# Optimization experiments

Hardware: AMD Instinct MI355X
Metric: run time of the kernel (lower is better)

## Reference

```python
import jax, jax.numpy as jnp
import numpy as np
import math

D = 2048            # fc_feat_size (hardcoded sqrt(2048) scale in source)
IMAGES = 20         # images_per_person
NEIGHBOR = 5        # neighbor_size (sliding window width)
T = IMAGES - NEIGHBOR + 1   # number of windows = 16
SCALE = 1.0 / math.sqrt(2048.0)


def _attention(x, Wq, bq, Wk, bk, Wv, bv):
    # x: [N, L, D] -> [N, L, D]; bmm-softmax-bmm as in source
    q = x @ Wq.T + bq
    k = x @ Wk.T + bk
    v = x @ Wv.T + bv
    dot = jnp.einsum('nld,nmd->nlm', q, k) * SCALE
    w = jax.nn.softmax(dot, axis=-1)
    return jnp.einsum('nlm,nmd->nld', w, v)


def _lstm_final(x, Wih, Whh, bih, bhh):
    # PyTorch-convention LSTM (gates i,f,g,o); x: [N, L, D] -> final hidden [N, H]
    N = x.shape[0]
    H = Whh.shape[1]
    xg = x @ Wih.T + (bih + bhh)   # [N, L, 4H] precompute input projections

    def step(carry, xt):
        h, c = carry
        gates = xt + h @ Whh.T
        i, f, g, o = jnp.split(gates, 4, axis=-1)
        c = jax.nn.sigmoid(f) * c + jax.nn.sigmoid(i) * jnp.tanh(g)
        h = jax.nn.sigmoid(o) * jnp.tanh(c)
        return (h, c), None

    init = (jnp.zeros((N, H), x.dtype), jnp.zeros((N, H), x.dtype))
    (h, _), _ = jax.lax.scan(step, init, jnp.swapaxes(xg, 0, 1))
    return h


def _layernorm(x, g, b, eps=1e-5):
    mu = jnp.mean(x, axis=-1, keepdims=True)
    var = jnp.var(x, axis=-1, keepdims=True)
    return (x - mu) * jax.lax.rsqrt(var + eps) * g + b


def setup_inputs() -> dict:
    key = jax.random.key(0)
    ks = iter(jax.random.split(key, 32))
    s = 0.02
    p = {}
    p['fc_feats'] = jax.random.normal(next(ks), (64, IMAGES, D), jnp.float32)
    for pre in ('nsa', 'sa'):
        for nm in ('Wq', 'Wk', 'Wv'):
            p[f'{pre}_{nm}'] = jax.random.normal(next(ks), (D, D), jnp.float32) * s
        for nm in ('bq', 'bk', 'bv'):
            p[f'{pre}_{nm}'] = jnp.zeros((D,), jnp.float32)
        p[f'{pre}_Wih'] = jax.random.normal(next(ks), (4 * D, D), jnp.float32) * s
        p[f'{pre}_Whh'] = jax.random.normal(next(ks), (4 * D, D), jnp.float32) * s
        p[f'{pre}_bih'] = jnp.zeros((4 * D,), jnp.float32)
        p[f'{pre}_bhh'] = jnp.zeros((4 * D,), jnp.float32)
    p['ln_g'] = jnp.ones((D,), jnp.float32)
    p['ln_b'] = jnp.zeros((D,), jnp.float32)
    return p


def reference(fc_feats,
              nsa_Wq, nsa_Wk, nsa_Wv, nsa_bq, nsa_bk, nsa_bv,
              nsa_Wih, nsa_Whh, nsa_bih, nsa_bhh,
              sa_Wq, sa_Wk, sa_Wv, sa_bq, sa_bk, sa_bv,
              sa_Wih, sa_Whh, sa_bih, sa_bhh,
              ln_g, ln_b):
    B = fc_feats.shape[0]
    # Sliding windows: window t covers images [t, t+NEIGHBOR) -> [B, T, W, D]
    idx = jnp.arange(T)[:, None] + jnp.arange(NEIGHBOR)[None, :]
    windows = fc_feats[:, idx]                       # [B, T, W, D]
    wflat = windows.reshape(B * T, NEIGHBOR, D)
    # NeighboringSelfAttention: attention within window + LSTM final state
    att = _attention(wflat, nsa_Wq, nsa_bq, nsa_Wk, nsa_bk, nsa_Wv, nsa_bv)
    nsa = _lstm_final(att, nsa_Wih, nsa_Whh, nsa_bih, nsa_bhh)  # [B*T, D]
    nsa_feats = nsa.reshape(B, T, D)
    new_nsa_feats = _layernorm(nsa_feats, ln_g, ln_b)
    # SelfAttention over the T window summaries + LSTM final state
    att2 = _attention(new_nsa_feats, sa_Wq, sa_bq, sa_Wk, sa_bk, sa_Wv, sa_bv)
    sa_feats = _lstm_final(att2, sa_Wih, sa_Whh, sa_bih, sa_bhh)  # [B, D]
    return (sa_feats, new_nsa_feats)
```

## Files before the change

### kernel.cpp

```cpp
#include <hip/hip_runtime.h>
#include <hip/hip_bf16.h>

typedef unsigned int  u32;
typedef unsigned short u16;

typedef __bf16 bf16x8 __attribute__((ext_vector_type(8)));
typedef float  f32x4  __attribute__((ext_vector_type(4)));

#define D2048 2048
#define SCALE 0.022097086912079612f

__device__ __forceinline__ u32 f2bfbits(float f) {
    u32 u = __float_as_uint(f);
    return (u + 0x7FFFu + ((u >> 16) & 1u)) >> 16;
}
__device__ __forceinline__ u32 pack2(float a, float b) {
    return f2bfbits(a) | (f2bfbits(b) << 16);
}
__device__ __forceinline__ float bf2f(u32 h) {
    return __uint_as_float(h << 16);
}
__device__ __forceinline__ void unpack8(uint4 v, float* f) {
    f[0] = bf2f(v.x & 0xFFFFu); f[1] = bf2f(v.x >> 16);
    f[2] = bf2f(v.y & 0xFFFFu); f[3] = bf2f(v.y >> 16);
// ... 6 lines not shown
    float e = __expf(2.f * x);
    return (e - 1.f) / (e + 1.f);
}

__device__ __forceinline__ void gload_lds16(const u16* g, u16* l) {
    __builtin_amdgcn_global_load_lds(
        (const __attribute__((address_space(1))) unsigned int*)g,
        (__attribute__((address_space(3))) unsigned int*)l,
        16, 0, 0);
}

struct CvtArgs {
    const float* src[8];
    u16*         dst[8];
    int          n4[8];
    int          nseg;
};
__global__ __launch_bounds__(256) void cvt_multi(CvtArgs a) {
    int stride = gridDim.x * 256;
    for (int s = 0; s < a.nseg; ++s) {
        const float4* S = reinterpret_cast<const float4*>(a.src[s]);
        uint2*        D = reinterpret_cast<uint2*>(a.dst[s]);
        int n4 = a.n4[s];
        for (int i = blockIdx.x * 256 + threadIdx.x; i < n4; i += stride) {
            float4 v = S[i];
            uint2 p;
            p.x = pack2(v.x, v.y);
            p.y = pack2(v.z, v.w);
            D[i] = p;
        }
    }
}

template <int SPLITK, bool OUT_BF16>
__global__ __launch_bounds__(512, 2) void gemm256(const u16* __restrict__ A, int lda,
                                                  const u16* __restrict__ B,
                                                  void* __restrict__ C0,
                                                  void* __restrict__ C1,
                                                  int M, int N, int K) {
    __shared__ u16 Ab[2][16384];
    __shared__ u16 Bb[2][16384];

    const int tid  = threadIdx.x;
    const int lane = tid & 63;
    const int wid  = tid >> 6;
    const int wm   = wid >> 2;
    const int wn   = wid & 3;
    const int l15  = lane & 15, l4 = lane >> 4;
    const int rowBase = blockIdx.y * 256;
    const int colBase = blockIdx.x * 256;
    const int kseg = K / SPLITK;
    const int kBeg = (SPLITK > 1) ? (int)blockIdx.z * kseg : 0;

    const int srow8 = lane >> 3;
    const int scw   = ((lane & 7) ^ srow8) * 8;
    const u16* gA = A + (size_t)(rowBase + wid * 8 + srow8) * lda + kBeg + scw;
    const u16* gB = B + (size_t)(colBase + wid * 8 + srow8) * (size_t)K + kBeg + scw;
    const int ldsW = wid * 512;

#define STAGE_A(buf, koff, q) \
    gload_lds16(gA + (size_t)((q) * 64) * lda + (koff), &Ab[buf][(q) * 4096 + ldsW])
#define STAGE_B(buf, koff, q) \
    gload_lds16(gB + (size_t)((q) * 64) * (size_t)K + (koff), &Bb[buf][(q) * 4096 + ldsW])

    f32x4 acc[8][4];
#pragma unroll
    for (int m = 0; m < 8; m++)
#pragma unroll
        for (int n = 0; n < 4; n++) acc[m][n] = f32x4{0.f, 0.f, 0.f, 0.f};

    const int nt = kseg >> 6;

#pragma unroll
    for (int q = 0; q < 4; ++q) { STAGE_A(0, 0, q); STAGE_B(0, 0, q); }

    const int swzA = (l15 & 7);

    for (int t = 0; t < nt; ++t) {
        const int cur = t & 1;
        const int nxt = cur ^ 1;
        const int kN  = (t + 1) << 6;
        const bool more = (t + 1 < nt);

        if (more) {
            STAGE_A(nxt, kN, 0);
            STAGE_A(nxt, kN, 1);
            asm volatile("s_waitcnt vmcnt(2)" ::: "memory");
        } else {
            asm volatile("s_waitcnt vmcnt(0)" ::: "memory");
        }
        __builtin_amdgcn_s_barrier();

        bf16x8 bfrag[4][2];
#pragma unroll
        for (int n = 0; n < 4; ++n)
#pragma unroll
            for (int kk = 0; kk < 2; ++kk)
                bfrag[n][kk] = *reinterpret_cast<const bf16x8*>(
                    &Bb[cur][(wn * 64 + n * 16 + l15) * 64 +
                             (((kk * 4 + l4) ^ swzA) * 8)]);

#pragma unroll
        for (int p = 0; p < 4; ++p) {
            bf16x8 afr[2][2];
#pragma unroll
            for (int mi = 0; mi < 2; ++mi)
#pragma unroll
                for (int kk = 0; kk < 2; ++kk)
                    afr[mi][kk] = *reinterpret_cast<const bf16x8*>(
                        &Ab[cur][(wm * 128 + (p * 2 + mi) * 16 + l15) * 64 +
                                 (((kk * 4 + l4) ^ swzA) * 8)]);
            if (more) {
                if (p == 0)      { STAGE_A(nxt, kN, 2); STAGE_A(nxt, kN, 3); }
                else if (p == 1) { STAGE_B(nxt, kN, 0); STAGE_B(nxt, kN, 1); }
                else if (p == 2) { STAGE_B(nxt, kN, 2); STAGE_B(nxt, kN, 3); }
            }
            __builtin_amdgcn_s_barrier();
            __builtin_amdgcn_sched_barrier(0);
            __builtin_amdgcn_s_setprio(1);
#pragma unroll
            for (int kk = 0; kk < 2; ++kk)
#pragma unroll
                for (int mi = 0; mi < 2; ++mi)
#pragma unroll
                    for (int n = 0; n < 4; ++n)
                        acc[p * 2 + mi][n] = __builtin_amdgcn_mfma_f32_16x16x32_bf16(
                            afr[mi][kk], bfrag[n][kk], acc[p * 2 + mi][n], 0, 0, 0);
            __builtin_amdgcn_s_setprio(0);
            __builtin_amdgcn_sched_barrier(0);
            __builtin_amdgcn_s_barrier();
        }
    }
#undef STAGE_A
#undef STAGE_B

    float* fdst = (SPLITK > 1 && blockIdx.z) ? (float*)C1 : (float*)C0;
#pragma unroll
    for (int m = 0; m < 8; ++m) {
        int row0 = rowBase + wm * 128 + m * 16 + l4 * 4;
#pragma unroll
        for (int n = 0; n < 4; ++n) {
            int col = colBase + wn * 64 + n * 16 + l15;
#pragma unroll
            for (int rr = 0; rr < 4; ++rr) {
                if (OUT_BF16)
                    ((u16*)C0)[(size_t)(row0 + rr) * N + col] = (u16)f2bfbits(acc[m][n][rr]);
                else
                    fdst[(size_t)(row0 + rr) * N + col] = acc[m][n][rr];
            }
        }
    }
}

template <bool QKV3, bool HAS_BIAS, bool OUT_BF16>
__global__ __launch_bounds__(256) void gemm_bt(const u16* __restrict__ A, int lda,
                                               const u16* __restrict__ B0,
                                               const u16* __restrict__ B1,
                                               const u16* __restrict__ B2,
                                               const float* __restrict__ bias0,
                                               const float* __restrict__ bias1,
                                               const float* __restrict__ bias2,
                                               void* __restrict__ Cout,
                                               size_t zCstride,
                                               int M, int N, int K) {
    __shared__ u16 Abuf[2][128 * 64];
    __shared__ u16 Bbuf[2][128 * 64];

    const int tid  = threadIdx.x;
    const int lane = tid & 63;
    const int wave = tid >> 6;
    const int wr   = (wave >> 1) * 64;
    const int wc   = (wave & 1) * 64;
    const int rowBase = blockIdx.y * 128;
    const int colBase = blockIdx.x * 128;
    const int l15 = lane & 15, l4 = lane >> 4;
    const int srow = lane >> 3;
    const int scol = (lane & 7) * 8;

    const u16* B = B0;
    const float* bias = bias0;
    void* C = Cout;
    if (QKV3) {
        int z = blockIdx.z;
        B    = (z == 0) ? B0 : ((z == 1) ? B1 : B2);
        bias = (z == 0) ? bias0 : ((z == 1) ? bias1 : bias2);
        C    = OUT_BF16 ? (void*)((u16*)Cout + (size_t)z * zCstride)
                        : (void*)((float*)Cout + (size_t)z * zCstride);
    }

    const u16* ga = A + (size_t)(rowBase + wave * 32 + srow) * lda + scol;
    const u16* gb = B + (size_t)(colBase + wave * 32 + srow) * K + scol;
    const int ldsOff = (wave * 32) * 64;

    f32x4 acc[4][4];
#pragma unroll
    for (int i = 0; i < 4; i++)
#pragma unroll
        for (int j = 0; j < 4; j++) acc[i][j] = f32x4{0.f, 0.f, 0.f, 0.f};

    const int nt = K >> 6;

#pragma unroll
    for (int i = 0; i < 4; ++i) {
        gload_lds16(ga + (size_t)(i * 8) * lda, &Abuf[0][ldsOff + i * 8 * 64]);
        gload_lds16(gb + (size_t)(i * 8) * K,   &Bbuf[0][ldsOff + i * 8 * 64]);
    }

    for (int t = 0; t < nt; ++t) {
        const int cur = t & 1;
        if (t + 1 < nt) {
            const int k1 = (t + 1) << 6;
#pragma unroll
            for (int i = 0; i < 4; ++i) {
                gload_lds16(ga + (size_t)(i * 8) * lda + k1,
                            &Abuf[cur ^ 1][ldsOff + i * 8 * 64]);
                gload_lds16(gb + (size_t)(i * 8) * K + k1,
                            &Bbuf[cur ^ 1][ldsOff + i * 8 * 64]);
            }
            asm volatile("s_waitcnt vmcnt(8)" ::: "memory");
        } else {
            asm volatile("s_waitcnt vmcnt(0)" ::: "memory");
        }
        __builtin_amdgcn_s_barrier();
        __builtin_amdgcn_sched_barrier(0);
#pragma unroll
        for (int kk = 0; kk < 2; ++kk) {
            bf16x8 af[4], bfr[4];
#pragma unroll
            for (int i = 0; i < 4; i++) {
                af[i]  = *reinterpret_cast<const bf16x8*>(
                    &Abuf[cur][(wr + i * 16 + l15) * 64 + kk * 32 + l4 * 8]);
                bfr[i] = *reinterpret_cast<const bf16x8*>(
                    &Bbuf[cur][(wc + i * 16 + l15) * 64 + kk * 32 + l4 * 8]);
            }
#pragma unroll
            for (int i = 0; i < 4; i++)
#pragma unroll
                for (int j = 0; j < 4; j++)
                    acc[i][j] = __builtin_amdgcn_mfma_f32_16x16x32_bf16(af[i], bfr[j],
                                                                        acc[i][j], 0, 0, 0);
        }
        __builtin_amdgcn_sched_barrier(0);
        __builtin_amdgcn_s_barrier();
    }

#pragma unroll
    for (int i = 0; i < 4; i++) {
        int row0 = rowBase + wr + i * 16 + l4 * 4;
#pragma unroll
        for (int j = 0; j < 4; j++) {
            int col = colBase + wc + j * 16 + l15;
            float bv = HAS_BIAS ? bias[col] : 0.f;
#pragma unroll
            for (int rr = 0; rr < 4; rr++) {
                float val = acc[i][j][rr] + bv;
                if (OUT_BF16)
                    ((u16*)C)[(size_t)(row0 + rr) * N + col] = (u16)f2bfbits(val);
                else
                    ((float*)C)[(size_t)(row0 + rr) * N + col] = val;
            }
        }
    }
}

__global__ __launch_bounds__(256) void gemm_skinny64(const u16* __restrict__ A,
                                                     const u16* __restrict__ B,
                                                     float* __restrict__ part,
                                                     int N, int K) {
    __shared__ u16 Abuf[2][64 * 64];
    __shared__ u16 Bbuf[2][128 * 64];
    const int tid = threadIdx.x, lane = tid & 63, wave = tid >> 6;
    const int colBase = blockIdx.x * 128;
    const int kp = blockIdx.y;
    const int kseg = K >> 3;
    const int kBeg = kp * kseg;
    const int l15 = lane & 15, l4 = lane >> 4;
    const int srow = lane >> 3, scol = (lane & 7) * 8;

    const u16* ga = A + (size_t)(wave * 16 + srow) * K + scol + kBeg;
    const u16* gb = B + (size_t)(colBase + wave * 32 + srow) * K + scol + kBeg;
    const int laOff = (wave * 16) * 64;
    const int lbOff = (wave * 32) * 64;

    f32x4 acc[4][2];
#pragma unroll
    for (int i = 0; i < 4; i++)
#pragma unroll
        for (int j = 0; j < 2; j++) acc[i][j] = f32x4{0.f, 0.f, 0.f, 0.f};

    const int nt = kseg >> 6;

#pragma unroll
    for (int i = 0; i < 2; ++i)
        gload_lds16(ga + (size_t)(i * 8) * K, &Abuf[0][laOff + i * 8 * 64]);
#pragma unroll
    for (int i = 0; i < 4; ++i)
        gload_lds16(gb + (size_t)(i * 8) * K, &Bbuf[0][lbOff + i * 8 * 64]);

    for (int t = 0; t < nt; ++t) {
        const int cur = t & 1;
        if (t + 1 < nt) {
            const int k1 = (t + 1) << 6;
#pragma unroll
            for (int i = 0; i < 2; ++i)
                gload_lds16(ga + (size_t)(i * 8) * K + k1, &Abuf[cur ^ 1][laOff + i * 8 * 64]);
#pragma unroll
            for (int i = 0; i < 4; ++i)
                gload_lds16(gb + (size_t)(i * 8) * K + k1, &Bbuf[cur ^ 1][lbOff + i * 8 * 64]);
            asm volatile("s_waitcnt vmcnt(6)" ::: "memory");
        } else {
            asm volatile("s_waitcnt vmcnt(0)" ::: "memory");
        }
        __builtin_amdgcn_s_barrier();
        __builtin_amdgcn_sched_barrier(0);
#pragma unroll
        for (int kk = 0; kk < 2; ++kk) {
            bf16x8 af[4], bfr[2];
#pragma unroll
            for (int i = 0; i < 4; i++)
                af[i] = *reinterpret_cast<const bf16x8*>(
                    &Abuf[cur][(i * 16 + l15) * 64 + kk * 32 + l4 * 8]);
#pragma unroll
            for (int j = 0; j < 2; j++)
                bfr[j] = *reinterpret_cast<const bf16x8*>(
                    &Bbuf[cur][(wave * 32 + j * 16 + l15) * 64 + kk * 32 + l4 * 8]);
#pragma unroll
            for (int i = 0; i < 4; i++)
#pragma unroll
                for (int j = 0; j < 2; j++)
                    acc[i][j] = __builtin_amdgcn_mfma_f32_16x16x32_bf16(af[i], bfr[j],
                                                                        acc[i][j], 0, 0, 0);
        }
        __builtin_amdgcn_sched_barrier(0);
        __builtin_amdgcn_s_barrier();
    }

    float* cp = part + (size_t)kp * 64 * N;
#pragma unroll
    for (int i = 0; i < 4; i++) {
        int row0 = i * 16 + l4 * 4;
#pragma unroll
        for (int j = 0; j < 2; j++) {
            int col = colBase + wave * 32 + j * 16 + l15;
#pragma unroll
            for (int rr = 0; rr < 4; rr++)
                cp[(size_t)(row0 + rr) * N + col] = acc[i][j][rr];
        }
    }
}

__global__ __launch_bounds__(256) void attn_win5(const u16* __restrict__ q0,
                                                 const u16* __restrict__ k0,
                                                 const u16* __restrict__ v0,
                                                 u16* __restrict__ att) {
    int n = blockIdx.x;
    int b = n >> 4, t = n & 15;
    int tid = threadIdx.x, lane = tid & 63, wave = tid >> 6;
    int d0 = tid * 8;
    size_t base = (size_t)(b * 20 + t) * D2048;

    float qv[5][8];
#pragma unroll
    for (int i = 0; i < 5; i++) {
        uint4 v = *reinterpret_cast<const uint4*>(q0 + base + (size_t)i * D2048 + d0);
        unpack8(v, qv[i]);
    }
    float part[25];
#pragma unroll
    for (int p = 0; p < 25; p++) part[p] = 0.f;
#pragma unroll
    for (int m = 0; m < 5; m++) {
        float kv[8];
        uint4 v = *reinterpret_cast<const uint4*>(k0 + base + (size_t)m * D2048 + d0);
        unpack8(v, kv);
#pragma unroll
        for (int l = 0; l < 5; l++)
#pragma unroll
            for (int j = 0; j < 8; j++) part[l * 5 + m] += qv[l][j] * kv[j];
    }
#pragma unroll
    for (int p = 0; p < 25; p++) {
// ... 99 lines not shown
        float dv[16], mx = -1e30f;
#pragma unroll
        for (int m = 0; m < 16; m++) {
            dv[m] = (wred[0][m] + wred[1][m] + wred[2][m] + wred[3][m]) * SCALE;
            mx = fmaxf(mx, dv[m]);
        }
        float ssum = 0.f;
#pragma unroll
        for (int m = 0; m < 16; m++) { dv[m] = __expf(dv[m] - mx); ssum += dv[m]; }
        float inv = 1.f / ssum;
#pragma unroll
        for (int m = 0; m < 16; m++) wmat[m] = dv[m] * inv;
    }
    __syncthreads();

    float oacc[8];
#pragma unroll
    for (int j = 0; j < 8; j++) oacc[j] = 0.f;
#pragma unroll
    for (int m = 0; m < 16; m++) {
        float vv[8];
        uint4 v = *reinterpret_cast<const uint4*>(v2 + kbase + (size_t)m * D2048 + d0);
        unpack8(v, vv);
        float w = wmat[m];
#pragma unroll
        for (int j = 0; j < 8; j++) oacc[j] += w * vv[j];
    }
    uint4 p;
    p.x = pack2(oacc[0], oacc[1]);
    p.y = pack2(oacc[2], oacc[3]);
    p.z = pack2(oacc[4], oacc[5]);
    p.w = pack2(oacc[6], oacc[7]);
    *reinterpret_cast<uint4*>(att2 + (size_t)r * D2048 + d0) = p;
}

template <int NPARTS>
__global__ __launch_bounds__(256) void lstm_gate(const u16* __restrict__ xg,
                                                 int xg_stride,
                                                 const float* __restrict__ hWa,
                                                 const float* __restrict__ hWb,
                                                 const float* __restrict__ bih,
                                                 const float* __restrict__ bhh,
                                                 float* __restrict__ c,
                                                 float* __restrict__ h,
                                                 u16* __restrict__ hbf,
                                                 float* __restrict__ hout,
                                                 int rows) {
    int idx = blockIdx.x * 256 + threadIdx.x;
    int total = rows * 512;
    if (idx >= total) return;
    int n  = idx >> 9;
    int j4 = (idx & 511) * 4;

    const u16* xr = xg + (size_t)n * xg_stride + j4;
    float4 gi, gf, gg, go;
    {
        uint2 ri = *reinterpret_cast<const uint2*>(xr);
        uint2 rf = *reinterpret_cast<const uint2*>(xr + 2048);
        uint2 rg = *reinterpret_cast<const uint2*>(xr + 4096);
        uint2 ro = *reinterpret_cast<const uint2*>(xr + 6144);
        gi = {bf2f(ri.x & 0xFFFFu), bf2f(ri.x >> 16), bf2f(ri.y & 0xFFFFu), bf2f(ri.y >> 16)};
        gf = {bf2f(rf.x & 0xFFFFu), bf2f(rf.x >> 16), bf2f(rf.y & 0xFFFFu), bf2f(rf.y >> 16)};
        gg = {bf2f(rg.x & 0xFFFFu), bf2f(rg.x >> 16), bf2f(rg.y & 0xFFFFu), bf2f(rg.y >> 16)};
        go = {bf2f(ro.x & 0xFFFFu), bf2f(ro.x >> 16), bf2f(ro.y & 0xFFFFu), bf2f(ro.y >> 16)};
    }

    float4 bi1 = *reinterpret_cast<const float4*>(bih + j4);
    float4 bf1 = *reinterpret_cast<const float4*>(bih + 2048 + j4);
    float4 bg1 = *reinterpret_cast<const float4*>(bih + 4096 + j4);
    float4 bo1 = *reinterpret_cast<const float4*>(bih + 6144 + j4);
    float4 bi2 = *reinterpret_cast<const float4*>(bhh + j4);
    float4 bf2_ = *reinterpret_cast<const float4*>(bhh + 2048 + j4);
    float4 bg2 = *reinterpret_cast<const float4*>(bhh + 4096 + j4);
    float4 bo2 = *reinterpret_cast<const float4*>(bhh + 6144 + j4);

    gi.x += bi1.x + bi2.x; gi.y += bi1.y + bi2.y; gi.z += bi1.z + bi2.z; gi.w += bi1.w + bi2.w;
    gf.x += bf1.x + bf2_.x; gf.y += bf1.y + bf2_.y; gf.z += bf1.z + bf2_.z; gf.w += bf1.w + bf2_.w;
    gg.x += bg1.x + bg2.x; gg.y += bg1.y + bg2.y; gg.z += bg1.z + bg2.z; gg.w += bg1.w + bg2.w;
    go.x += bo1.x + bo2.x; go.y += bo1.y + bo2.y; go.z += bo1.z + bo2.z; go.w += bo1.w + bo2.w;

#pragma unroll
    for (int p = 0; p < NPARTS; ++p) {
        const float* hr = (NPARTS == 2)
            ? ((p == 0 ? hWa : hWb) + (size_t)n * 8192)
            : (hWa + (size_t)p * 524288 + (size_t)n * 8192);
        float4 hi = *reinterpret_cast<const float4*>(hr + j4);
        float4 hf = *reinterpret_cast<const float4*>(hr + 2048 + j4);
        float4 hg = *reinterpret_cast<const float4*>(hr + 4096 + j4);
        float4 ho = *reinterpret_cast<const float4*>(hr + 6144 + j4);
        gi.x += hi.x; gi.y += hi.y; gi.z += hi.z; gi.w += hi.w;
        gf.x += hf.x; gf.y += hf.y; gf.z += hf.z; gf.w += hf.w;
        gg.x += hg.x; gg.y += hg.y; gg.z += hg.z; gg.w += hg.w;
        go.x += ho.x; go.y += ho.y; go.z += ho.z; go.w += ho.w;
    }
    float4 cc;
    if (NPARTS == 0) { cc.x = cc.y = cc.z = cc.w = 0.f; }
    else             cc = *reinterpret_cast<const float4*>(c + (size_t)n * 2048 + j4);

    float cx = sigmf(gf.x) * cc.x + sigmf(gi.x) * tanhf_(gg.x);
    float cy = sigmf(gf.y) * cc.y + sigmf(gi.y) * tanhf_(gg.y);
    float cz = sigmf(gf.z) * cc.z + sigmf(gi.z) * tanhf_(gg.z);
    float cw = sigmf(gf.w) * cc.w + sigmf(gi.w) * tanhf_(gg.w);
    float hx = sigmf(go.x) * tanhf_(cx);
    float hy = sigmf(go.y) * tanhf_(cy);
    float hz = sigmf(go.z) * tanhf_(cz);
    float hw_ = sigmf(go.w) * tanhf_(cw);

    float4 co = {cx, cy, cz, cw};
    float4 ho_ = {hx, hy, hz, hw_};
    *reinterpret_cast<float4*>(c + (size_t)n * 2048 + j4) = co;
    *reinterpret_cast<float4*>(h + (size_t)n * 2048 + j4) = ho_;
    uint2 hp;
    hp.x = pack2(hx, hy);
    hp.y = pack2(hz, hw_);
    *reinterpret_cast<uint2*>(hbf + (size_t)n * 2048 + j4) = hp;
    if (hout) *reinterpret_cast<float4*>(hout + (size_t)n * 2048 + j4) = ho_;
}

__global__ __launch_bounds__(256) void layernorm_k(const float* __restrict__ x,
                                                   const float* __restrict__ g,
                                                   const float* __restrict__ b,
                                                   float* __restrict__ y,
                                                   u16* __restrict__ ybf) {
    int row = blockIdx.x;
    int tid = threadIdx.x, lane = tid & 63, wave = tid >> 6;
    const float* xr = x + (size_t)row * D2048;
    int j = tid * 8;
    float4 v1 = *reinterpret_cast<const float4*>(xr + j);
    float4 v2 = *reinterpret_cast<const float4*>(xr + j + 4);
    float s  = v1.x + v1.y + v1.z + v1.w + v2.x + v2.y + v2.z + v2.w;
    float s2 = v1.x * v1.x + v1.y * v1.y + v1.z * v1.z + v1.w * v1.w +
               v2.x * v2.x + v2.y * v2.y + v2.z * v2.z + v2.w * v2.w;
#pragma unroll
    for (int msk = 32; msk; msk >>= 1) {
        s  += __shfl_xor(s, msk, 64);
        s2 += __shfl_xor(s2, msk, 64);
    }
    __shared__ float red[4][2];
    if (lane == 0) { red[wave][0] = s; red[wave][1] = s2; }
    __syncthreads();
    s  = red[0][0] + red[1][0] + red[2][0] + red[3][0];
    s2 = red[0][1] + red[1][1] + red[2][1] + red[3][1];
    float mu  = s * (1.f / 2048.f);
    float var = s2 * (1.f / 2048.f) - mu * mu;
    float rs  = __frsqrt_rn(var + 1e-5f);

    float4 g1 = *reinterpret_cast<const float4*>(g + j);
    float4 g2 = *reinterpret_cast<const float4*>(g + j + 4);
    float4 b1 = *reinterpret_cast<const float4*>(b + j);
    float4 b2 = *reinterpret_cast<const float4*>(b + j + 4);
    float o[8];
    o[0] = (v1.x - mu) * rs * g1.x + b1.x;
    o[1] = (v1.y - mu) * rs * g1.y + b1.y;
    o[2] = (v1.z - mu) * rs * g1.z + b1.z;
    o[3] = (v1.w - mu) * rs * g1.w + b1.w;
    o[4] = (v2.x - mu) * rs * g2.x + b2.x;
    o[5] = (v2.y - mu) * rs * g2.y + b2.y;
    o[6] = (v2.z - mu) * rs * g2.z + b2.z;
    o[7] = (v2.w - mu) * rs * g2.w + b2.w;
    float4 o1 = {o[0], o[1], o[2], o[3]};
    float4 o2 = {o[4], o[5], o[6], o[7]};
    float* yr = y + (size_t)row * D2048;
    *reinterpret_cast<float4*>(yr + j)     = o1;
    *reinterpret_cast<float4*>(yr + j + 4) = o2;
    uint4 p;
    p.x = pack2(o[0], o[1]);
    p.y = pack2(o[2], o[3]);
    p.z = pack2(o[4], o[5]);
    p.w = pack2(o[6], o[7]);
    *reinterpret_cast<uint4*>(ybf + (size_t)row * D2048 + j) = p;
}

static inline void launch_qkv(hipStream_t s, const u16* A, const u16* Wq,
                              const u16* Wk, const u16* Wv, const float* bq,
                              const float* bk, const float* bv, u16* out,
                              int M, int N, int K) {
    dim3 grid(N / 128, M / 128, 3);
    gemm_bt<true, true, true><<<grid, 256, 0, s>>>(A, K, Wq, Wk, Wv, bq, bk, bv,
                                                   out, (size_t)M * N, M, N, K);
}

extern "C" void kernel_launch(void* const* d_in, const int* in_sizes, int n_in,
                              void* d_out, int out_size, void* d_ws, size_t ws_size,
                              hipStream_t stream) {
    const float* fc      = (const float*)d_in[0];
    const float* nsa_Wq  = (const float*)d_in[1];
    const float* nsa_Wk  = (const float*)d_in[2];
    const float* nsa_Wv  = (const float*)d_in[3];
    const float* nsa_bq  = (const float*)d_in[4];
    const float* nsa_bk  = (const float*)d_in[5];
    const float* nsa_bv  = (const float*)d_in[6];
    const float* nsa_Wih = (const float*)d_in[7];
    const float* nsa_Whh = (const float*)d_in[8];
    const float* nsa_bih = (const float*)d_in[9];
    const float* nsa_bhh = (const float*)d_in[10];
    const float* sa_Wq   = (const float*)d_in[11];
    const float* sa_Wk   = (const float*)d_in[12];
    const float* sa_Wv   = (const float*)d_in[13];
    const float* sa_bq   = (const float*)d_in[14];
    const float* sa_bk   = (const float*)d_in[15];
    const float* sa_bv   = (const float*)d_in[16];
    const float* sa_Wih  = (const float*)d_in[17];
    const float* sa_Whh  = (const float*)d_in[18];
    const float* sa_bih  = (const float*)d_in[19];
    const float* sa_bhh  = (const float*)d_in[20];
    const float* ln_g    = (const float*)d_in[21];
    const float* ln_b    = (const float*)d_in[22];

    float* outF   = (float*)d_out;
    float* out_sa = outF;
    float* out_ln = outF + 131072;

    char* W = (char*)d_ws;
    u16* W_q   = (u16*)(W + 0);
    u16* W_k   = (u16*)(W + 8388608);
    u16* W_v   = (u16*)(W + 16777216);
    u16* W_ih  = (u16*)(W + 25165824);
    u16* W_hh1 = (u16*)(W + 58720256);
    u16* W_hh2 = (u16*)(W + 92274688);
    u16*   Xbf  = (u16*)(W + 125829120);
    u16*   q0   = (u16*)(W + 131072000);
    u16*   att1 = (u16*)(W + 146800640);
    u16*   xg   = (u16*)(W + 167772160);
    float* h1   = (float*)(W + 0);
    float* c1   = (float*)(W + 8388608);
    u16*   h1bf = (u16*)(W + 16777216);
    float* partA = (float*)(W + 131072000);
    float* partB = (float*)(W + 25165824);
    u16*   lnbf = Xbf;
    u16*   q2   = q0;
    u16*   att2 = att1;
    float* hW2  = (float*)(W + 131072000);
    float* h2   = (float*)(W + 147849216);
    float* c2   = (float*)(W + 148373504);
    u16*   h2bf = (u16*)(W + 148897792);

    {
        CvtArgs a{};
        a.src[0] = fc;      a.dst[0] = Xbf;   a.n4[0] = 655360;
        a.src[1] = nsa_Wq;  a.dst[1] = W_q;   a.n4[1] = 1048576;
        a.src[2] = nsa_Wk;  a.dst[2] = W_k;   a.n4[2] = 1048576;
        a.src[3] = nsa_Wv;  a.dst[3] = W_v;   a.n4[3] = 1048576;
        a.src[4] = nsa_Wih; a.dst[4] = W_ih;  a.n4[4] = 4194304;
        a.src[5] = nsa_Whh; a.dst[5] = W_hh1; a.n4[5] = 4194304;
        a.src[6] = sa_Whh;  a.dst[6] = W_hh2; a.n4[6] = 4194304;
        a.nseg = 7;
        cvt_multi<<<2048, 256, 0, stream>>>(a);
    }

    launch_qkv(stream, Xbf, W_q, W_k, W_v, nsa_bq, nsa_bk, nsa_bv, q0, 1280, 2048, 2048);

    attn_win5<<<1024, 256, 0, stream>>>(q0, q0 + 2621440, q0 + 5242880, att1);

    gemm256<1, true><<<dim3(32, 20, 1), 512, 0, stream>>>(att1, 2048, W_ih,
                                                          xg, nullptr, 5120, 8192, 2048);

    lstm_gate<0><<<2048, 256, 0, stream>>>(xg, 40960, nullptr, nullptr, nsa_bih,
                                           nsa_bhh, c1, h1, h1bf, nullptr, 1024);
    for (int t = 1; t < 5; ++t) {
        gemm256<2, false><<<dim3(32, 4, 2), 512, 0, stream>>>(h1bf, 2048, W_hh1,
                                                              partA, partB, 1024, 8192, 2048);
        lstm_gate<2><<<2048, 256, 0, stream>>>(xg + (size_t)t * 8192, 40960, partA,
                                               partB, nsa_bih, nsa_bhh, c1, h1, h1bf,
                                               nullptr, 1024);
    }

    layernorm_k<<<1024, 256, 0, stream>>>(h1, ln_g, ln_b, out_ln, lnbf);

    {
        CvtArgs a{};
        a.src[0] = sa_Wq;  a.dst[0] = W_q;  a.n4[0] = 1048576;
        a.src[1] = sa_Wk;  a.dst[1] = W_k;  a.n4[1] = 1048576;
        a.src[2] = sa_Wv;  a.dst[2] = W_v;  a.n4[2] = 1048576;
        a.src[3] = sa_Wih; a.dst[3] = W_ih; a.n4[3] = 4194304;
        a.nseg = 4;
        cvt_multi<<<2048, 256, 0, stream>>>(a);
    }

    launch_qkv(stream, lnbf, W_q, W_k, W_v, sa_bq, sa_bk, sa_bv, q2, 1024, 2048, 2048);

    attn_seq16<<<1024, 256, 0, stream>>>(q2, q2 + 2097152, q2 + 4194304, att2);

    gemm256<1, true><<<dim3(32, 4, 1), 512, 0, stream>>>(att2, 2048, W_ih,
                                                         xg, nullptr, 1024, 8192, 2048);

    lstm_gate<0><<<128, 256, 0, stream>>>(xg, 131072, nullptr, nullptr, sa_bih,
                                          sa_bhh, c2, h2, h2bf, nullptr, 64);
    for (int t = 1; t < 16; ++t) {
        gemm_skinny64<<<dim3(64, 8), 256, 0, stream>>>(h2bf, W_hh2, hW2, 8192, 2048);
        lstm_gate<8><<<128, 256, 0, stream>>>(xg + (size_t)t * 8192, 131072, hW2,
                                              nullptr, sa_bih, sa_bhh, c2, h2, h2bf,
                                              (t == 15) ? out_sa : nullptr, 64);
    }
}
```

Measured before the change: 1.030 ms.

## Fuse LSTM recurrent GEMM with gate activation using gate-interleaved weight tiles

```diff
diff --git a/kernel.cpp b/kernel.cpp
--- a/kernel.cpp
+++ b/kernel.cpp
@@ -62,11 +62,10 @@
     }
 }
 
-template <int SPLITK, bool OUT_BF16>
+template <bool OUT_BF16>
 __global__ __launch_bounds__(512, 2) void gemm256(const u16* __restrict__ A, int lda,
                                                   const u16* __restrict__ B,
                                                   void* __restrict__ C0,
-                                                  void* __restrict__ C1,
                                                   int M, int N, int K) {
     __shared__ u16 Ab[2][16384];
     __shared__ u16 Bb[2][16384];
@@ -79,13 +78,11 @@
     const int l15  = lane & 15, l4 = lane >> 4;
     const int rowBase = blockIdx.y * 256;
     const int colBase = blockIdx.x * 256;
-    const int kseg = K / SPLITK;
-    const int kBeg = (SPLITK > 1) ? (int)blockIdx.z * kseg : 0;
 
     const int srow8 = lane >> 3;
     const int scw   = ((lane & 7) ^ srow8) * 8;
-    const u16* gA = A + (size_t)(rowBase + wid * 8 + srow8) * lda + kBeg + scw;
-    const u16* gB = B + (size_t)(colBase + wid * 8 + srow8) * (size_t)K + kBeg + scw;
+    const u16* gA = A + (size_t)(rowBase + wid * 8 + srow8) * lda + scw;
+    const u16* gB = B + (size_t)(colBase + wid * 8 + srow8) * (size_t)K + scw;
     const int ldsW = wid * 512;
 
 #define STAGE_A(buf, koff, q) \
@@ -99,7 +96,7 @@
 #pragma unroll
         for (int n = 0; n < 4; n++) acc[m][n] = f32x4{0.f, 0.f, 0.f, 0.f};
 
-    const int nt = kseg >> 6;
+    const int nt = K >> 6;
 
 #pragma unroll
     for (int q = 0; q < 4; ++q) { STAGE_A(0, 0, q); STAGE_B(0, 0, q); }
@@ -164,7 +161,6 @@
 #undef STAGE_A
 #undef STAGE_B
 
-    float* fdst = (SPLITK > 1 && blockIdx.z) ? (float*)C1 : (float*)C0;
 #pragma unroll
     for (int m = 0; m < 8; ++m) {
         int row0 = rowBase + wm * 128 + m * 16 + l4 * 4;
@@ -176,23 +172,22 @@
                 if (OUT_BF16)
                     ((u16*)C0)[(size_t)(row0 + rr) * N + col] = (u16)f2bfbits(acc[m][n][rr]);
                 else
-                    fdst[(size_t)(row0 + rr) * N + col] = acc[m][n][rr];
+                    ((float*)C0)[(size_t)(row0 + rr) * N + col] = acc[m][n][rr];
             }
         }
     }
 }
 
-template <bool QKV3, bool HAS_BIAS, bool OUT_BF16>
-__global__ __launch_bounds__(256) void gemm_bt(const u16* __restrict__ A, int lda,
-                                               const u16* __restrict__ B0,
-                                               const u16* __restrict__ B1,
-                                               const u16* __restrict__ B2,
-                                               const float* __restrict__ bias0,
-                                               const float* __restrict__ bias1,
-                                               const float* __restrict__ bias2,
-                                               void* __restrict__ Cout,
-                                               size_t zCstride,
-                                               int M, int N, int K) {
+__global__ __launch_bounds__(256) void gemm_qkv(const u16* __restrict__ A,
+                                                const u16* __restrict__ B0,
+                                                const u16* __restrict__ B1,
+                                                const u16* __restrict__ B2,
+                                                const float* __restrict__ bias0,
+                                                const float* __restrict__ bias1,
+                                                const float* __restrict__ bias2,
+                                                u16* __restrict__ Cout,
+                                                size_t zCstride,
+                                                int M, int N, int K) {
     __shared__ u16 Abuf[2][128 * 64];
     __shared__ u16 Bbuf[2][128 * 64];
 
@@ -207,18 +202,12 @@
     const int srow = lane >> 3;
     const int scol = (lane & 7) * 8;
 
-    const u16* B = B0;
-    const float* bias = bias0;
-    void* C = Cout;
-    if (QKV3) {
-        int z = blockIdx.z;
-        B    = (z == 0) ? B0 : ((z == 1) ? B1 : B2);
-        bias = (z == 0) ? bias0 : ((z == 1) ? bias1 : bias2);
-        C    = OUT_BF16 ? (void*)((u16*)Cout + (size_t)z * zCstride)
-                        : (void*)((float*)Cout + (size_t)z * zCstride);
-    }
-
-    const u16* ga = A + (size_t)(rowBase + wave * 32 + srow) * lda + scol;
+    const int z = blockIdx.z;
+    const u16* B      = (z == 0) ? B0 : ((z == 1) ? B1 : B2);
+    const float* bias = (z == 0) ? bias0 : ((z == 1) ? bias1 : bias2);
+    u16* C = Cout + (size_t)z * zCstride;
+
+    const u16* ga = A + (size_t)(rowBase + wave * 32 + srow) * K + scol;
     const u16* gb = B + (size_t)(colBase + wave * 32 + srow) * K + scol;
     const int ldsOff = (wave * 32) * 64;
 
@@ -232,8 +221,8 @@
 
 #pragma unroll
     for (int i = 0; i < 4; ++i) {
-        gload_lds16(ga + (size_t)(i * 8) * lda, &Abuf[0][ldsOff + i * 8 * 64]);
-        gload_lds16(gb + (size_t)(i * 8) * K,   &Bbuf[0][ldsOff + i * 8 * 64]);
+        gload_lds16(ga + (size_t)(i * 8) * K, &Abuf[0][ldsOff + i * 8 * 64]);
+        gload_lds16(gb + (size_t)(i * 8) * K, &Bbuf[0][ldsOff + i * 8 * 64]);
     }
 
     for (int t = 0; t < nt; ++t) {
@@ -242,7 +231,7 @@
             const int k1 = (t + 1) << 6;
 #pragma unroll
             for (int i = 0; i < 4; ++i) {
-                gload_lds16(ga + (size_t)(i * 8) * lda + k1,
+                gload_lds16(ga + (size_t)(i * 8) * K + k1,
                             &Abuf[cur ^ 1][ldsOff + i * 8 * 64]);
                 gload_lds16(gb + (size_t)(i * 8) * K + k1,
                             &Bbuf[cur ^ 1][ldsOff + i * 8 * 64]);
@@ -280,35 +269,162 @@
 #pragma unroll
         for (int j = 0; j < 4; j++) {
             int col = colBase + wc + j * 16 + l15;
-            float bv = HAS_BIAS ? bias[col] : 0.f;
-#pragma unroll
-            for (int rr = 0; rr < 4; rr++) {
-                float val = acc[i][j][rr] + bv;
-                if (OUT_BF16)
-                    ((u16*)C)[(size_t)(row0 + rr) * N + col] = (u16)f2bfbits(val);
-                else
-                    ((float*)C)[(size_t)(row0 + rr) * N + col] = val;
-            }
-        }
-    }
-}
-
-__global__ __launch_bounds__(256) void gemm_skinny64(const u16* __restrict__ A,
-                                                     const u16* __restrict__ B,
-                                                     float* __restrict__ part,
-                                                     int N, int K) {
-    __shared__ u16 Abuf[2][64 * 64];
-    __shared__ u16 Bbuf[2][128 * 64];
+            float bv = bias[col];
+#pragma unroll
+            for (int rr = 0; rr < 4; rr++)
+                C[(size_t)(row0 + rr) * N + col] = (u16)f2bfbits(acc[i][j][rr] + bv);
+        }
+    }
+}
+
+template <bool LAST>
+__global__ __launch_bounds__(256) void gemm_gate128(
+    const u16* __restrict__ A,
+    const u16* __restrict__ B,
+    const u16* __restrict__ xg,
+    int xg_stride,
+    const float* __restrict__ bih,
+    const float* __restrict__ bhh,
+    float* __restrict__ c,
+    u16* __restrict__ hbf_out,
+    float* __restrict__ hf,
+    int K) {
+    __shared__ u16 smem[32768];
+    u16* Ab = smem;
+    u16* Bb = smem + 16384;
+
     const int tid = threadIdx.x, lane = tid & 63, wave = tid >> 6;
-    const int colBase = blockIdx.x * 128;
-    const int kp = blockIdx.y;
-    const int kseg = K >> 3;
-    const int kBeg = kp * kseg;
+    const int wr = (wave >> 1) * 64, wc = (wave & 1) * 64;
     const int l15 = lane & 15, l4 = lane >> 4;
     const int srow = lane >> 3, scol = (lane & 7) * 8;
-
-    const u16* ga = A + (size_t)(wave * 16 + srow) * K + scol + kBeg;
-    const u16* gb = B + (size_t)(colBase + wave * 32 + srow) * K + scol + kBeg;
+    const int jBase = blockIdx.x * 32;
+    const int rowBase = blockIdx.y * 128;
+
+    const u16* ga = A + (size_t)(rowBase + wave * 32 + srow) * K + scol;
+    const u16* gb[4];
+#pragma unroll
+    for (int i = 0; i < 4; ++i) {
+        int lc = wave * 32 + i * 8 + srow;
+        int br = jBase + (lc & 31) + (lc >> 5) * 2048;
+        gb[i] = B + (size_t)br * K + scol;
+    }
+    const int ldsOff = (wave * 32) * 64;
+
+    f32x4 acc[4][4];
+#pragma unroll
+    for (int i = 0; i < 4; i++)
+#pragma unroll
+        for (int j = 0; j < 4; j++) acc[i][j] = f32x4{0.f, 0.f, 0.f, 0.f};
+
+    const int nt = K >> 6;
+#pragma unroll
+    for (int i = 0; i < 4; ++i) {
+        gload_lds16(ga + (size_t)(i * 8) * K, &Ab[ldsOff + i * 8 * 64]);
+        gload_lds16(gb[i], &Bb[ldsOff + i * 8 * 64]);
+    }
+
+    for (int t = 0; t < nt; ++t) {
+        const int cur = (t & 1) * 8192;
+        if (t + 1 < nt) {
+            const int k1 = (t + 1) << 6;
+            const int nxt = ((t + 1) & 1) * 8192;
+#pragma unroll
+            for (int i = 0; i < 4; ++i) {
+                gload_lds16(ga + (size_t)(i * 8) * K + k1, &Ab[nxt + ldsOff + i * 8 * 64]);
+                gload_lds16(gb[i] + k1, &Bb[nxt + ldsOff + i * 8 * 64]);
+            }
+            asm volatile("s_waitcnt vmcnt(8)" ::: "memory");
+        } else {
+            asm volatile("s_waitcnt vmcnt(0)" ::: "memory");
+        }
+        __builtin_amdgcn_s_barrier();
+        __builtin_amdgcn_sched_barrier(0);
+#pragma unroll
+        for (int kk = 0; kk < 2; ++kk) {
+            bf16x8 af[4], bfr[4];
+#pragma unroll
+            for (int i = 0; i < 4; i++) {
+                af[i]  = *reinterpret_cast<const bf16x8*>(
+                    &Ab[cur + (wr + i * 16 + l15) * 64 + kk * 32 + l4 * 8]);
+                bfr[i] = *reinterpret_cast<const bf16x8*>(
+                    &Bb[cur + (wc + i * 16 + l15) * 64 + kk * 32 + l4 * 8]);
+            }
+#pragma unroll
+            for (int i = 0; i < 4; i++)
+#pragma unroll
+                for (int j = 0; j < 4; j++)
+                    acc[i][j] = __builtin_amdgcn_mfma_f32_16x16x32_bf16(af[i], bfr[j],
+                                                                        acc[i][j], 0, 0, 0);
+        }
+        __builtin_amdgcn_sched_barrier(0);
+        __builtin_amdgcn_s_barrier();
+    }
+
+    float* Cs = (float*)smem;
+#pragma unroll
+    for (int i = 0; i < 4; i++)
+#pragma unroll
+        for (int j = 0; j < 4; j++)
+#pragma unroll
+            for (int rr = 0; rr < 4; rr++)
+                Cs[(wr + i * 16 + l4 * 4 + rr) * 128 + (wc + j * 16 + l15)] =
+                    acc[i][j][rr];
+    __syncthreads();
+
+    const int j  = tid & 31;
+    const int rb = tid >> 5;
+    const int gj = jBase + j;
+    const float bi_ = bih[gj]        + bhh[gj];
+    const float bf_ = bih[gj + 2048] + bhh[gj + 2048];
+    const float bg_ = bih[gj + 4096] + bhh[gj + 4096];
+    const float bo_ = bih[gj + 6144] + bhh[gj + 6144];
+#pragma unroll
+    for (int k = 0; k < 16; ++k) {
+        int r = rb * 16 + k;
+        int n = rowBase + r;
+        const u16* xr = xg + (size_t)n * xg_stride;
+        float gi = Cs[r * 128 + j]      + bf2f((u32)xr[gj])        + bi_;
+        float gf = Cs[r * 128 + 32 + j] + bf2f((u32)xr[gj + 2048]) + bf_;
+        float gg = Cs[r * 128 + 64 + j] + bf2f((u32)xr[gj + 4096]) + bg_;
+        float go = Cs[r * 128 + 96 + j] + bf2f((u32)xr[gj + 6144]) + bo_;
+        size_t idx = (size_t)n * 2048 + gj;
+        float cc = c[idx];
+        float cn = sigmf(gf) * cc + sigmf(gi) * tanhf_(gg);
+        float hn = sigmf(go) * tanhf_(cn);
+        c[idx] = cn;
+        hbf_out[idx] = (u16)f2bfbits(hn);
+        if (LAST) hf[idx] = hn;
+    }
+}
+
+__global__ __launch_bounds__(256) void gemm_gate64(
+    const u16* __restrict__ A,
+    const u16* __restrict__ B,
+    const u16* __restrict__ xg,
+    int xg_stride,
+    const float* __restrict__ bih,
+    const float* __restrict__ bhh,
+    float* __restrict__ c,
+    u16* __restrict__ hbf_out,
+    float* __restrict__ hf,
+    int K) {
+    __shared__ u16 smem[24576];
+    u16* Ab = smem;
+    u16* Bb = smem + 8192;
+
+    const int tid = threadIdx.x, lane = tid & 63, wave = tid >> 6;
+    const int l15 = lane & 15, l4 = lane >> 4;
+    const int srow = lane >> 3, scol = (lane & 7) * 8;
+    const int jBase = blockIdx.x * 32;
+
+    const u16* ga = A + (size_t)(wave * 16 + srow) * K + scol;
+    const u16* gb[4];
+#pragma unroll
+    for (int i = 0; i < 4; ++i) {
+        int lc = wave * 32 + i * 8 + srow;
+        int br = jBase + (lc & 31) + (lc >> 5) * 2048;
+        gb[i] = B + (size_t)br * K + scol;
+    }
     const int laOff = (wave * 16) * 64;
     const int lbOff = (wave * 32) * 64;
 
@@ -318,25 +434,27 @@
 #pragma unroll
         for (int j = 0; j < 2; j++) acc[i][j] = f32x4{0.f, 0.f, 0.f, 0.f};
 
-    const int nt = kseg >> 6;
-
+    const int nt = K >> 6;
 #pragma unroll
     for (int i = 0; i < 2; ++i)
-        gload_lds16(ga + (size_t)(i * 8) * K, &Abuf[0][laOff + i * 8 * 64]);
+        gload_lds16(ga + (size_t)(i * 8) * K, &Ab[laOff + i * 8 * 64]);
 #pragma unroll
     for (int i = 0; i < 4; ++i)
-        gload_lds16(gb + (size_t)(i * 8) * K, &Bbuf[0][lbOff + i * 8 * 64]);
+        gload_lds16(gb[i], &Bb[lbOff + i * 8 * 64]);
 
     for (int t = 0; t < nt; ++t) {
-        const int cur = t & 1;
+        const int curA = (t & 1) * 4096;
+        const int curB = (t & 1) * 8192;
         if (t + 1 < nt) {
             const int k1 = (t + 1) << 6;
+            const int nxA = ((t + 1) & 1) * 4096;
+            const int nxB = ((t + 1) & 1) * 8192;
 #pragma unroll
             for (int i = 0; i < 2; ++i)
-                gload_lds16(ga + (size_t)(i * 8) * K + k1, &Abuf[cur ^ 1][laOff + i * 8 * 64]);
+                gload_lds16(ga + (size_t)(i * 8) * K + k1, &Ab[nxA + laOff + i * 8 * 64]);
 #pragma unroll
             for (int i = 0; i < 4; ++i)
-                gload_lds16(gb + (size_t)(i * 8) * K + k1, &Bbuf[cur ^ 1][lbOff + i * 8 * 64]);
+                gload_lds16(gb[i] + k1, &Bb[nxB + lbOff + i * 8 * 64]);
             asm volatile("s_waitcnt vmcnt(6)" ::: "memory");
         } else {
             asm volatile("s_waitcnt vmcnt(0)" ::: "memory");
@@ -349,11 +467,11 @@
 #pragma unroll
             for (int i = 0; i < 4; i++)
                 af[i] = *reinterpret_cast<const bf16x8*>(
-                    &Abuf[cur][(i * 16 + l15) * 64 + kk * 32 + l4 * 8]);
+                    &Ab[curA + (i * 16 + l15) * 64 + kk * 32 + l4 * 8]);
 #pragma unroll
             for (int j = 0; j < 2; j++)
                 bfr[j] = *reinterpret_cast<const bf16x8*>(
-                    &Bbuf[cur][(wave * 32 + j * 16 + l15) * 64 + kk * 32 + l4 * 8]);
+                    &Bb[curB + (wave * 32 + j * 16 + l15) * 64 + kk * 32 + l4 * 8]);
 #pragma unroll
             for (int i = 0; i < 4; i++)
 #pragma unroll
@@ -365,18 +483,91 @@
         __builtin_amdgcn_s_barrier();
     }
 
-    float* cp = part + (size_t)kp * 64 * N;
-#pragma unroll
-    for (int i = 0; i < 4; i++) {
-        int row0 = i * 16 + l4 * 4;
-#pragma unroll
-        for (int j = 0; j < 2; j++) {
-            int col = colBase + wave * 32 + j * 16 + l15;
+    float* Cs = (float*)smem;
+#pragma unroll
+    for (int i = 0; i < 4; i++)
+#pragma unroll
+        for (int j = 0; j < 2; j++)
 #pragma unroll
             for (int rr = 0; rr < 4; rr++)
-                cp[(size_t)(row0 + rr) * N + col] = acc[i][j][rr];
-        }
-    }
+                Cs[(i * 16 + l4 * 4 + rr) * 128 + (wave * 32 + j * 16 + l15)] =
+                    acc[i][j][rr];
+    __syncthreads();
+
+    const int j  = tid & 31;
+    const int rb = tid >> 5;
+    const int gj = jBase + j;
+    const float bi_ = bih[gj]        + bhh[gj];
+    const float bf_ = bih[gj + 2048] + bhh[gj + 2048];
+    const float bg_ = bih[gj + 4096] + bhh[gj + 4096];
+    const float bo_ = bih[gj + 6144] + bhh[gj + 6144];
+#pragma unroll
+    for (int k = 0; k < 8; ++k) {
+        int n = rb * 8 + k;
+        const u16* xr = xg + (size_t)n * xg_stride;
+        float gi = Cs[n * 128 + j]      + bf2f((u32)xr[gj])        + bi_;
+        float gf = Cs[n * 128 + 32 + j] + bf2f((u32)xr[gj + 2048]) + bf_;
+        float gg = Cs[n * 128 + 64 + j] + bf2f((u32)xr[gj + 4096]) + bg_;
+        float go = Cs[n * 128 + 96 + j] + bf2f((u32)xr[gj + 6144]) + bo_;
+        size_t idx = (size_t)n * 2048 + gj;
+        float cc = c[idx];
+        float cn = sigmf(gf) * cc + sigmf(gi) * tanhf_(gg);
+        float hn = sigmf(go) * tanhf_(cn);
+        c[idx] = cn;
+        hbf_out[idx] = (u16)f2bfbits(hn);
+        if (hf) hf[idx] = hn;
+    }
+}
+
+__global__ __launch_bounds__(256) void lstm_gate0(const u16* __restrict__ xg,
+                                                  int xg_stride,
+                                                  const float* __restrict__ bih,
+                                                  const float* __restrict__ bhh,
+                                                  float* __restrict__ c,
+                                                  u16* __restrict__ hbf,
+                                                  int rows) {
+    int idx = blockIdx.x * 256 + threadIdx.x;
+    int total = rows * 512;
+    if (idx >= total) return;
+    int n  = idx >> 9;
+    int j4 = (idx & 511) * 4;
+
+    const u16* xr = xg + (size_t)n * xg_stride + j4;
+    float4 gi, gf, gg, go;
+    {
+        uint2 ri = *reinterpret_cast<const uint2*>(xr);
+        uint2 rg = *reinterpret_cast<const uint2*>(xr + 4096);
+        uint2 ro = *reinterpret_cast<const uint2*>(xr + 6144);
+        gi = {bf2f(ri.x & 0xFFFFu), bf2f(ri.x >> 16), bf2f(ri.y & 0xFFFFu), bf2f(ri.y >> 16)};
+        gg = {bf2f(rg.x & 0xFFFFu), bf2f(rg.x >> 16), bf2f(rg.y & 0xFFFFu), bf2f(rg.y >> 16)};
+        go = {bf2f(ro.x & 0xFFFFu), bf2f(ro.x >> 16), bf2f(ro.y & 0xFFFFu), bf2f(ro.y >> 16)};
+    }
+    float4 bi1 = *reinterpret_cast<const float4*>(bih + j4);
+    float4 bg1 = *reinterpret_cast<const float4*>(bih + 4096 + j4);
+    float4 bo1 = *reinterpret_cast<const float4*>(bih + 6144 + j4);
+    float4 bi2 = *reinterpret_cast<const float4*>(bhh + j4);
+    float4 bg2 = *reinterpret_cast<const float4*>(bhh + 4096 + j4);
+    float4 bo2 = *reinterpret_cast<const float4*>(bhh + 6144 + j4);
+
+    gi.x += bi1.x + bi2.x; gi.y += bi1.y + bi2.y; gi.z += bi1.z + bi2.z; gi.w += bi1.w + bi2.w;
+    gg.x += bg1.x + bg2.x; gg.y += bg1.y + bg2.y; gg.z += bg1.z + bg2.z; gg.w += bg1.w + bg2.w;
+    go.x += bo1.x + bo2.x; go.y += bo1.y + bo2.y; go.z += bo1.z + bo2.z; go.w += bo1.w + bo2.w;
+
+    float cx = sigmf(gi.x) * tanhf_(gg.x);
+    float cy = sigmf(gi.y) * tanhf_(gg.y);
+    float cz = sigmf(gi.z) * tanhf_(gg.z);
+    float cw = sigmf(gi.w) * tanhf_(gg.w);
+    float hx = sigmf(go.x) * tanhf_(cx);
+    float hy = sigmf(go.y) * tanhf_(cy);
+    float hz = sigmf(go.z) * tanhf_(cz);
+    float hw_ = sigmf(go.w) * tanhf_(cw);
+
+    float4 co = {cx, cy, cz, cw};
+    *reinterpret_cast<float4*>(c + (size_t)n * 2048 + j4) = co;
+    uint2 hp;
+    hp.x = pack2(hx, hy);
+    hp.y = pack2(hz, hw_);
+    *reinterpret_cast<uint2*>(hbf + (size_t)n * 2048 + j4) = hp;
 }
 
 __global__ __launch_bounds__(256) void attn_win5(const u16* __restrict__ q0,
@@ -542,89 +733,6 @@
     p.z = pack2(oacc[4], oacc[5]);
     p.w = pack2(oacc[6], oacc[7]);
     *reinterpret_cast<uint4*>(att2 + (size_t)r * D2048 + d0) = p;
-}
-
-template <int NPARTS>
-__global__ __launch_bounds__(256) void lstm_gate(const u16* __restrict__ xg,
-                                                 int xg_stride,
-                                                 const float* __restrict__ hWa,
-                                                 const float* __restrict__ hWb,
-                                                 const float* __restrict__ bih,
-                                                 const float* __restrict__ bhh,
-                                                 float* __restrict__ c,
-                                                 float* __restrict__ h,
-                                                 u16* __restrict__ hbf,
-                                                 float* __restrict__ hout,
-                                                 int rows) {
-    int idx = blockIdx.x * 256 + threadIdx.x;
-    int total = rows * 512;
-    if (idx >= total) return;
-    int n  = idx >> 9;
-    int j4 = (idx & 511) * 4;
-
-    const u16* xr = xg + (size_t)n * xg_stride + j4;
-    float4 gi, gf, gg, go;
-    {
-        uint2 ri = *reinterpret_cast<const uint2*>(xr);
-        uint2 rf = *reinterpret_cast<const uint2*>(xr + 2048);
-        uint2 rg = *reinterpret_cast<const uint2*>(xr + 4096);
-        uint2 ro = *reinterpret_cast<const uint2*>(xr + 6144);
-        gi = {bf2f(ri.x & 0xFFFFu), bf2f(ri.x >> 16), bf2f(ri.y & 0xFFFFu), bf2f(ri.y >> 16)};
-        gf = {bf2f(rf.x & 0xFFFFu), bf2f(rf.x >> 16), bf2f(rf.y & 0xFFFFu), bf2f(rf.y >> 16)};
-        gg = {bf2f(rg.x & 0xFFFFu), bf2f(rg.x >> 16), bf2f(rg.y & 0xFFFFu), bf2f(rg.y >> 16)};
-        go = {bf2f(ro.x & 0xFFFFu), bf2f(ro.x >> 16), bf2f(ro.y & 0xFFFFu), bf2f(ro.y >> 16)};
-    }
-
-    float4 bi1 = *reinterpret_cast<const float4*>(bih + j4);
-    float4 bf1 = *reinterpret_cast<const float4*>(bih + 2048 + j4);
-    float4 bg1 = *reinterpret_cast<const float4*>(bih + 4096 + j4);
-    float4 bo1 = *reinterpret_cast<const float4*>(bih + 6144 + j4);
-    float4 bi2 = *reinterpret_cast<const float4*>(bhh + j4);
-    float4 bf2_ = *reinterpret_cast<const float4*>(bhh + 2048 + j4);
-    float4 bg2 = *reinterpret_cast<const float4*>(bhh + 4096 + j4);
-    float4 bo2 = *reinterpret_cast<const float4*>(bhh + 6144 + j4);
-
-    gi.x += bi1.x + bi2.x; gi.y += bi1.y + bi2.y; gi.z += bi1.z + bi2.z; gi.w += bi1.w + bi2.w;
-    gf.x += bf1.x + bf2_.x; gf.y += bf1.y + bf2_.y; gf.z += bf1.z + bf2_.z; gf.w += bf1.w + bf2_.w;
-    gg.x += bg1.x + bg2.x; gg.y += bg1.y + bg2.y; gg.z += bg1.z + bg2.z; gg.w += bg1.w + bg2.w;
-    go.x += bo1.x + bo2.x; go.y += bo1.y + bo2.y; go.z += bo1.z + bo2.z; go.w += bo1.w + bo2.w;
-
-#pragma unroll
-    for (int p = 0; p < NPARTS; ++p) {
-        const float* hr = (NPARTS == 2)
-            ? ((p == 0 ? hWa : hWb) + (size_t)n * 8192)
-            : (hWa + (size_t)p * 524288 + (size_t)n * 8192);
-        float4 hi = *reinterpret_cast<const float4*>(hr + j4);
-        float4 hf = *reinterpret_cast<const float4*>(hr + 2048 + j4);
-        float4 hg = *reinterpret_cast<const float4*>(hr + 4096 + j4);
-        float4 ho = *reinterpret_cast<const float4*>(hr + 6144 + j4);
-        gi.x += hi.x; gi.y += hi.y; gi.z += hi.z; gi.w += hi.w;
-        gf.x += hf.x; gf.y += hf.y; gf.z += hf.z; gf.w += hf.w;
-        gg.x += hg.x; gg.y += hg.y; gg.z += hg.z; gg.w += hg.w;
-        go.x += ho.x; go.y += ho.y; go.z += ho.z; go.w += ho.w;
-    }
-    float4 cc;
-    if (NPARTS == 0) { cc.x = cc.y = cc.z = cc.w = 0.f; }
-    else             cc = *reinterpret_cast<const float4*>(c + (size_t)n * 2048 + j4);
-
-    float cx = sigmf(gf.x) * cc.x + sigmf(gi.x) * tanhf_(gg.x);
-    float cy = sigmf(gf.y) * cc.y + sigmf(gi.y) * tanhf_(gg.y);
-    float cz = sigmf(gf.z) * cc.z + sigmf(gi.z) * tanhf_(gg.z);
-    float cw = sigmf(gf.w) * cc.w + sigmf(gi.w) * tanhf_(gg.w);
-    float hx = sigmf(go.x) * tanhf_(cx);
-    float hy = sigmf(go.y) * tanhf_(cy);
-    float hz = sigmf(go.z) * tanhf_(cz);
-    float hw_ = sigmf(go.w) * tanhf_(cw);
-
-    float4 co = {cx, cy, cz, cw};
-    float4 ho_ = {hx, hy, hz, hw_};
-    *reinterpret_cast<float4*>(c + (size_t)n * 2048 + j4) = co;
-    *reinterpret_cast<float4*>(h + (size_t)n * 2048 + j4) = ho_;
-    uint2 hp;
-    hp.x = pack2(hx, hy);
-    hp.y = pack2(hz, hw_);
-    *reinterpret_cast<uint2*>(hbf + (size_t)n * 2048 + j4) = hp;
-    if (hout) *reinterpret_cast<float4*>(hout + (size_t)n * 2048 + j4) = ho_;
 }
 
 __global__ __launch_bounds__(256) void layernorm_k(const float* __restrict__ x,
@@ -686,8 +794,8 @@
                               const float* bk, const float* bv, u16* out,
                               int M, int N, int K) {
     dim3 grid(N / 128, M / 128, 3);
-    gemm_bt<true, true, true><<<grid, 256, 0, s>>>(A, K, Wq, Wk, Wv, bq, bk, bv,
-                                                   out, (size_t)M * N, M, N, K);
+    gemm_qkv<<<grid, 256, 0, s>>>(A, Wq, Wk, Wv, bq, bk, bv, out,
+                                  (size_t)M * N, M, N, K);
 }
 
 extern "C" void kernel_launch(void* const* d_in, const int* in_sizes, int n_in,
@@ -732,18 +840,16 @@
     u16*   q0   = (u16*)(W + 131072000);
     u16*   att1 = (u16*)(W + 146800640);
     u16*   xg   = (u16*)(W + 167772160);
-    float* h1   = (float*)(W + 0);
-    float* c1   = (float*)(W + 8388608);
-    u16*   h1bf = (u16*)(W + 16777216);
-    float* partA = (float*)(W + 131072000);
-    float* partB = (float*)(W + 25165824);
-    u16*   lnbf = Xbf;
-    u16*   q2   = q0;
-    u16*   att2 = att1;
-    float* hW2  = (float*)(W + 131072000);
-    float* h2   = (float*)(W + 147849216);
-    float* c2   = (float*)(W + 148373504);
-    u16*   h2bf = (u16*)(W + 148897792);
+    float* h1    = (float*)(W + 0);
+    float* c1    = (float*)(W + 8388608);
+    u16*   hbfA  = (u16*)(W + 16777216);
+    u16*   hbfB  = (u16*)(W + 131072000);
+    u16*   lnbf  = Xbf;
+    u16*   q2    = q0;
+    u16*   att2  = att1;
+    float* c2    = (float*)(W + 148373504);
+    u16*   h2bfA = (u16*)(W + 148897792);
+    u16*   h2bfB = (u16*)(W + 149422080);
 
     {
         CvtArgs a{};
@@ -762,17 +868,24 @@
 
     attn_win5<<<1024, 256, 0, stream>>>(q0, q0 + 2621440, q0 + 5242880, att1);
 
-    gemm256<1, true><<<dim3(32, 20, 1), 512, 0, stream>>>(att1, 2048, W_ih,
-                                                          xg, nullptr, 5120, 8192, 2048);
-
-    lstm_gate<0><<<2048, 256, 0, stream>>>(xg, 40960, nullptr, nullptr, nsa_bih,
-                                           nsa_bhh, c1, h1, h1bf, nullptr, 1024);
-    for (int t = 1; t < 5; ++t) {
-        gemm256<2, false><<<dim3(32, 4, 2), 512, 0, stream>>>(h1bf, 2048, W_hh1,
-                                                              partA, partB, 1024, 8192, 2048);
-        lstm_gate<2><<<2048, 256, 0, stream>>>(xg + (size_t)t * 8192, 40960, partA,
-                                               partB, nsa_bih, nsa_bhh, c1, h1, h1bf,
-                                               nullptr, 1024);
+    gemm256<true><<<dim3(32, 20), 512, 0, stream>>>(att1, 2048, W_ih, xg,
+                                                    5120, 8192, 2048);
+
+    lstm_gate0<<<2048, 256, 0, stream>>>(xg, 40960, nsa_bih, nsa_bhh, c1, hbfA, 1024);
+    {
+        u16* hin = hbfA;
+        for (int t = 1; t < 5; ++t) {
+            u16* hout = (t & 1) ? hbfB : hbfA;
+            if (t == 4)
+                gemm_gate128<true><<<dim3(64, 8), 256, 0, stream>>>(
+                    hin, W_hh1, xg + (size_t)t * 8192, 40960, nsa_bih, nsa_bhh,
+                    c1, hout, h1, 2048);
+            else
+                gemm_gate128<false><<<dim3(64, 8), 256, 0, stream>>>(
+                    hin, W_hh1, xg + (size_t)t * 8192, 40960, nsa_bih, nsa_bhh,
+                    c1, hout, nullptr, 2048);
+            hin = hout;
+        }
     }
 
     layernorm_k<<<1024, 256, 0, stream>>>(h1, ln_g, ln_b, out_ln, lnbf);
@@ -791,15 +904,18 @@
 
     attn_seq16<<<1024, 256, 0, stream>>>(q2, q2 + 2097152, q2 + 4194304, att2);
 
-    gemm256<1, true><<<dim3(32, 4, 1), 512, 0, stream>>>(att2, 2048, W_ih,
-                                                         xg, nullptr, 1024, 8192, 2048);
-
-    lstm_gate<0><<<128, 256, 0, stream>>>(xg, 131072, nullptr, nullptr, sa_bih,
-                                          sa_bhh, c2, h2, h2bf, nullptr, 64);
-    for (int t = 1; t < 16; ++t) {
-        gemm_skinny64<<<dim3(64, 8), 256, 0, stream>>>(h2bf, W_hh2, hW2, 8192, 2048);
-        lstm_gate<8><<<128, 256, 0, stream>>>(xg + (size_t)t * 8192, 131072, hW2,
-                                              nullptr, sa_bih, sa_bhh, c2, h2, h2bf,
-                                              (t == 15) ? out_sa : nullptr, 64);
-    }
-}
+    gemm256<true><<<dim3(32, 4), 512, 0, stream>>>(att2, 2048, W_ih, xg,
+                                                   1024, 8192, 2048);
+
+    lstm_gate0<<<128, 256, 0, stream>>>(xg, 131072, sa_bih, sa_bhh, c2, h2bfA, 64);
+    {
+        u16* hin = h2bfA;
+        for (int t = 1; t < 16; ++t) {
+            u16* hout = (t & 1) ? h2bfB : h2bfA;
+            gemm_gate64<<<dim3(64), 256, 0, stream>>>(
+                hin, W_hh2, xg + (size_t)t * 8192, 131072, sa_bih, sa_bhh,
+                c2, hout, (t == 15) ? out_sa : nullptr, 2048);
+            hin = hout;
+        }
+    }
+}
```

Measured after the change: 1.171 ms. 13.7% more time.
